# Optimization experiments

Measured on AMD Instinct MI355X. Metric: run time of the kernel, lower is better.

The kernel has to match this reference:

```python
import jax, jax.numpy as jnp
import numpy as np

N = 100000   # number of orientation vectors
MUL = 128    # multiplicity per output irrep


def _cg_tensors():
    # Clebsch-Gordan (wigner-3j style) tensors for 1o x 1o -> 0e, 1e, 2e
    # l=1 basis in e3nn real-SH order: index 0=y, 1=z, 2=x
    Y, Z, X = 0, 1, 2
    # l_out = 0: identity / sqrt(3)
    c0 = np.zeros((3, 3, 1), np.float32)
    for i in range(3):
        c0[i, i, 0] = 1.0 / np.sqrt(3.0)
    # l_out = 1: Levi-Civita / sqrt(6) (cyclic in (y,z,x) = cyclic in (x,y,z))
    c1 = np.zeros((3, 3, 3), np.float32)
    s = 1.0 / np.sqrt(6.0)
    for (i, j, k) in [(0, 1, 2), (1, 2, 0), (2, 0, 1)]:
        c1[i, j, k] = s
        c1[j, i, k] = -s
    # l_out = 2: symmetric traceless part, m = -2..2 -> (xy, yz, 2z^2-x^2-y^2, zx, x^2-y^2)
    a = 1.0 / np.sqrt(10.0)
    c2 = np.zeros((3, 3, 5), np.float32)
    c2[X, Y, 0] = c2[Y, X, 0] = a
    c2[Y, Z, 1] = c2[Z, Y, 1] = a
    c2[Z, Z, 2] = 2.0 * a / np.sqrt(3.0)
    c2[Y, Y, 2] = -a / np.sqrt(3.0)
    c2[X, X, 2] = -a / np.sqrt(3.0)
    c2[Z, X, 3] = c2[X, Z, 3] = a
    c2[X, X, 4] = a
    c2[Y, Y, 4] = -a
    return jnp.asarray(c0), jnp.asarray(c1), jnp.asarray(c2)

_CG = _cg_tensors()
# e3nn path weights: irrep_normalization='component', path_normalization='element'
# -> alpha = (2*l_out+1) / (mul1*mul2) = 2l+1, coefficient = sqrt(alpha)
_PW = (1.0, 3.0 ** 0.5, 5.0 ** 0.5)


def setup_inputs() -> dict:
    key = jax.random.key(0)
    k1, k2 = jax.random.split(key)
    ori = jax.random.normal(k1, (N, 3), dtype=jnp.float32)
    weights = jax.random.normal(k2, (3 * MUL,), dtype=jnp.float32)
    return {"ori": ori, "weights": weights}


def reference(ori, weights):
    # TensorProduct(1o, 1o -> 128x0e+128x1e+128x2e), 'uvw' paths, shared weights.
    w = weights.reshape(3, MUL)  # one (1,1,MUL) weight block per path
    n = ori.shape[0]
    outs = []
    for p, (cg, pw) in enumerate(zip(_CG, _PW)):
        t = jnp.einsum('ni,nj,ijk->nk', ori, ori, cg)      # [N, 2l+1]
        blk = pw * jnp.einsum('nk,w->nwk', t, w[p])        # [N, MUL, 2l+1]
        outs.append(blk.reshape(n, -1))
    return jnp.concatenate(outs, axis=-1)  # [N, MUL*(1+3+5)]
```

## Files before the change

kernel.cpp:

```cpp
#include <hip/hip_runtime.h>


#define THREADS 256
#define CPR 144
#define GRID 2016
#define RPT 28

__global__ __launch_bounds__(THREADS) void ori_embed_kernel(
    const float* __restrict__ ori,
    const float* __restrict__ weights,
    float* __restrict__ out,
    int n_rows)
{
    const int tid = blockIdx.x * THREADS + threadIdx.x;
    const int c = tid % CPR;
    const int g = tid / CPR;
    const int r0 = g * RPT;

    float coef[8];
    int sel[8];
#pragma unroll
    for (int i = 0; i < 8; ++i) {
        const int col = (i < 4) ? (4 * c + i) : (576 + 4 * c + (i - 4));
        if (col < 128)      { coef[i] = weights[col];  sel[i] = 0; }
        else if (col < 512) { coef[i] = 0.0f;          sel[i] = 0; }
        else { const int j = col - 512;
               coef[i] = weights[256 + j / 5];         sel[i] = 1 + j % 5; }
    }

    float4* __restrict__ out4 = reinterpret_cast<float4*>(out);

    if (r0 + RPT <= n_rows) {
        union { float4 v[RPT * 3 / 4]; float f[RPT * 3]; } d;
        const float4* __restrict__ src =
            reinterpret_cast<const float4*>(ori + 3 * (size_t)r0);
#pragma unroll
        for (int k = 0; k < RPT * 3 / 4; ++k) d.v[k] = src[k];

#pragma unroll
        for (int j = 0; j < RPT; ++j) {
            const float vy = d.f[3 * j + 0];
            const float vz = d.f[3 * j + 1];
            const float vx = d.f[3 * j + 2];
            const float xx = vx * vx, yy = vy * vy, zz = vz * vz;
            const float s0 = (xx + yy + zz) * 0.57735026918962576f;
            const float s1 = 1.41421356237309505f * (vx * vy);
            const float s2 = 1.41421356237309505f * (vy * vz);
            const float s3 = 0.40824829046386302f * (2.0f * zz - xx - yy);
            const float s4 = 1.41421356237309505f * (vz * vx);
            const float s5 = 0.70710678118654752f * (xx - yy);

            float r[8];
#pragma unroll
            for (int i = 0; i < 8; ++i) {
                float t = s0;
                t = (sel[i] == 1) ? s1 : t;
                t = (sel[i] == 2) ? s2 : t;
                t = (sel[i] == 3) ? s3 : t;
                t = (sel[i] == 4) ? s4 : t;
                t = (sel[i] == 5) ? s5 : t;
                r[i] = coef[i] * t;
            }
            const size_t base = (size_t)(r0 + j) * (2 * CPR) + c;
            out4[base]       = make_float4(r[0], r[1], r[2], r[3]);
            out4[base + CPR] = make_float4(r[4], r[5], r[6], r[7]);
        }
    } else {
        for (int j = 0; r0 + j < n_rows; ++j) {
            const int n = r0 + j;
            const float vy = ori[3 * n + 0];
            const float vz = ori[3 * n + 1];
            const float vx = ori[3 * n + 2];
            const float xx = vx * vx, yy = vy * vy, zz = vz * vz;
            const float s0 = (xx + yy + zz) * 0.57735026918962576f;
            const float s1 = 1.41421356237309505f * (vx * vy);
            const float s2 = 1.41421356237309505f * (vy * vz);
            const float s3 = 0.40824829046386302f * (2.0f * zz - xx - yy);
            const float s4 = 1.41421356237309505f * (vz * vx);
            const float s5 = 0.70710678118654752f * (xx - yy);

            float r[8];
#pragma unroll
            for (int i = 0; i < 8; ++i) {
                float t = s0;
                t = (sel[i] == 1) ? s1 : t;
                t = (sel[i] == 2) ? s2 : t;
                t = (sel[i] == 3) ? s3 : t;
                t = (sel[i] == 4) ? s4 : t;
                t = (sel[i] == 5) ? s5 : t;
                r[i] = coef[i] * t;
            }
            const size_t base = (size_t)n * (2 * CPR) + c;
            out4[base]       = make_float4(r[0], r[1], r[2], r[3]);
            out4[base + CPR] = make_float4(r[4], r[5], r[6], r[7]);
        }
    }
}

extern "C" void kernel_launch(void* const* d_in, const int* in_sizes, int n_in,
                              void* d_out, int out_size, void* d_ws, size_t ws_size,
                              hipStream_t stream) {
    const float* ori = (const float*)d_in[0];
    const float* weights = (const float*)d_in[1];
    float* out = (float*)d_out;
    const int n_rows = in_sizes[0] / 3;

    hipLaunchKernelGGL(ori_embed_kernel, dim3(GRID), dim3(THREADS), 0, stream,
                       ori, weights, out, n_rows);
}
```

Measured before the change: 93.38 us.

## Software-pipeline input loads in batches and double rows per thread group

Each thread group now handles 56 rows instead of 28, processed in batches of 8 rows. The next batch's input is prefetched into registers while the current batch computes and stores. This halves the grid and adds a launch-bounds occupancy hint, with the aim of lowering register pressure from the large unrolled load and overlapping reads with the write stream. The kernel is dominated by output writes, so the gain may be small, and fewer, larger groups risk load imbalance or lower parallelism.

```diff
diff --git a/kernel.cpp b/kernel.cpp
--- a/kernel.cpp
+++ b/kernel.cpp
@@ -3,10 +3,38 @@
 
 #define THREADS 256
 #define CPR 144
-#define GRID 2016
-#define RPT 28
+#define GRID 1017
+#define BATCH 8
+#define NB 7
+#define RPG (BATCH * NB)
 
-__global__ __launch_bounds__(THREADS) void ori_embed_kernel(
+__device__ __forceinline__ void emit_row(float4* __restrict__ out4, int n, int c,
+                                         float vy, float vz, float vx,
+                                         const float coef[8], const int sel[8]) {
+    const float xx = vx * vx, yy = vy * vy, zz = vz * vz;
+    const float s0 = (xx + yy + zz) * 0.57735026918962576f;
+    const float s1 = 1.41421356237309505f * (vx * vy);
+    const float s2 = 1.41421356237309505f * (vy * vz);
+    const float s3 = 0.40824829046386302f * (2.0f * zz - xx - yy);
+    const float s4 = 1.41421356237309505f * (vz * vx);
+    const float s5 = 0.70710678118654752f * (xx - yy);
+    float r[8];
+#pragma unroll
+    for (int i = 0; i < 8; ++i) {
+        float t = s0;
+        t = (sel[i] == 1) ? s1 : t;
+        t = (sel[i] == 2) ? s2 : t;
+        t = (sel[i] == 3) ? s3 : t;
+        t = (sel[i] == 4) ? s4 : t;
+        t = (sel[i] == 5) ? s5 : t;
+        r[i] = coef[i] * t;
+    }
+    const size_t ob = (size_t)n * (2 * CPR) + c;
+    out4[ob]       = make_float4(r[0], r[1], r[2], r[3]);
+    out4[ob + CPR] = make_float4(r[4], r[5], r[6], r[7]);
+}
+
+__global__ __launch_bounds__(THREADS, 4) void ori_embed_kernel(
     const float* __restrict__ ori,
     const float* __restrict__ weights,
     float* __restrict__ out,
@@ -15,7 +43,8 @@
     const int tid = blockIdx.x * THREADS + threadIdx.x;
     const int c = tid % CPR;
     const int g = tid / CPR;
-    const int r0 = g * RPT;
+    const int r0 = g * RPG;
+    if (r0 >= n_rows) return;
 
     float coef[8];
     int sel[8];
@@ -29,71 +58,39 @@
     }
 
     float4* __restrict__ out4 = reinterpret_cast<float4*>(out);
+    const float4* __restrict__ src = reinterpret_cast<const float4*>(ori);
 
-    if (r0 + RPT <= n_rows) {
-        union { float4 v[RPT * 3 / 4]; float f[RPT * 3]; } d;
-        const float4* __restrict__ src =
-            reinterpret_cast<const float4*>(ori + 3 * (size_t)r0);
+    const int nb = min(NB, (n_rows - r0) / BATCH);
+    const int base = 42 * g;
+
+    float4 cur[6], nxt[6];
+    if (nb > 0) {
 #pragma unroll
-        for (int k = 0; k < RPT * 3 / 4; ++k) d.v[k] = src[k];
+        for (int k = 0; k < 6; ++k) cur[k] = src[base + k];
+    }
+    for (int b = 0; b < nb; ++b) {
+        const bool more = (b + 1 < nb);
+        if (more) {
+#pragma unroll
+            for (int k = 0; k < 6; ++k) nxt[k] = src[base + 6 * (b + 1) + k];
+        }
+        const float* f = reinterpret_cast<const float*>(cur);
+        const int rb = r0 + b * BATCH;
+#pragma unroll
+        for (int j = 0; j < BATCH; ++j) {
+            emit_row(out4, rb + j, c, f[3 * j + 0], f[3 * j + 1], f[3 * j + 2],
+                     coef, sel);
+        }
+        if (more) {
+#pragma unroll
+            for (int k = 0; k < 6; ++k) cur[k] = nxt[k];
+        }
+    }
 
-#pragma unroll
-        for (int j = 0; j < RPT; ++j) {
-            const float vy = d.f[3 * j + 0];
-            const float vz = d.f[3 * j + 1];
-            const float vx = d.f[3 * j + 2];
-            const float xx = vx * vx, yy = vy * vy, zz = vz * vz;
-            const float s0 = (xx + yy + zz) * 0.57735026918962576f;
-            const float s1 = 1.41421356237309505f * (vx * vy);
-            const float s2 = 1.41421356237309505f * (vy * vz);
-            const float s3 = 0.40824829046386302f * (2.0f * zz - xx - yy);
-            const float s4 = 1.41421356237309505f * (vz * vx);
-            const float s5 = 0.70710678118654752f * (xx - yy);
-
-            float r[8];
-#pragma unroll
-            for (int i = 0; i < 8; ++i) {
-                float t = s0;
-                t = (sel[i] == 1) ? s1 : t;
-                t = (sel[i] == 2) ? s2 : t;
-                t = (sel[i] == 3) ? s3 : t;
-                t = (sel[i] == 4) ? s4 : t;
-                t = (sel[i] == 5) ? s5 : t;
-                r[i] = coef[i] * t;
-            }
-            const size_t base = (size_t)(r0 + j) * (2 * CPR) + c;
-            out4[base]       = make_float4(r[0], r[1], r[2], r[3]);
-            out4[base + CPR] = make_float4(r[4], r[5], r[6], r[7]);
-        }
-    } else {
-        for (int j = 0; r0 + j < n_rows; ++j) {
-            const int n = r0 + j;
-            const float vy = ori[3 * n + 0];
-            const float vz = ori[3 * n + 1];
-            const float vx = ori[3 * n + 2];
-            const float xx = vx * vx, yy = vy * vy, zz = vz * vz;
-            const float s0 = (xx + yy + zz) * 0.57735026918962576f;
-            const float s1 = 1.41421356237309505f * (vx * vy);
-            const float s2 = 1.41421356237309505f * (vy * vz);
-            const float s3 = 0.40824829046386302f * (2.0f * zz - xx - yy);
-            const float s4 = 1.41421356237309505f * (vz * vx);
-            const float s5 = 0.70710678118654752f * (xx - yy);
-
-            float r[8];
-#pragma unroll
-            for (int i = 0; i < 8; ++i) {
-                float t = s0;
-                t = (sel[i] == 1) ? s1 : t;
-                t = (sel[i] == 2) ? s2 : t;
-                t = (sel[i] == 3) ? s3 : t;
-                t = (sel[i] == 4) ? s4 : t;
-                t = (sel[i] == 5) ? s5 : t;
-                r[i] = coef[i] * t;
-            }
-            const size_t base = (size_t)n * (2 * CPR) + c;
-            out4[base]       = make_float4(r[0], r[1], r[2], r[3]);
-            out4[base + CPR] = make_float4(r[4], r[5], r[6], r[7]);
-        }
+    const int rend = min(r0 + RPG, n_rows);
+    for (int n = r0 + nb * BATCH; n < rend; ++n) {
+        emit_row(out4, n, c, ori[3 * n + 0], ori[3 * n + 1], ori[3 * n + 2],
+                 coef, sel);
     }
 }
 
```

Result: no change. 94.20 us (+0.9%).

## Stage output tiles in double-buffered LDS for fully contiguous streaming stores

Applied to the files above, without the earlier changes.

Output rows are now built in a double-buffered shared-memory tile of 8 rows by 288 float4 chunks. The block then copies each tile to global memory as one contiguous span, so consecutive threads write consecutive float4s. Each block processes 25 tiles, and computing the next tile overlaps with storing the current one. The goal is more coalesced, sequential write traffic in this store-bound kernel. The cost is extra LDS traffic, a barrier per tile, scalar per-thread loads of ori, and a serial tail loop in the last block.

```diff
diff --git a/kernel.cpp b/kernel.cpp
--- a/kernel.cpp
+++ b/kernel.cpp
@@ -1,10 +1,12 @@
 #include <hip/hip_runtime.h>
 
 
-#define THREADS 256
-#define CPR 144
-#define GRID 2016
-#define RPT 28
+#define THREADS 576
+#define GRID 512
+#define TPB 25
+#define TROWS 8
+#define CPRow 288
+#define TCHUNKS (TROWS * CPRow)
 
 __global__ __launch_bounds__(THREADS) void ori_embed_kernel(
     const float* __restrict__ ori,
@@ -12,16 +14,17 @@
     float* __restrict__ out,
     int n_rows)
 {
-    const int tid = blockIdx.x * THREADS + threadIdx.x;
-    const int c = tid % CPR;
-    const int g = tid / CPR;
-    const int r0 = g * RPT;
+    __shared__ float4 lds[2][TCHUNKS];
 
-    float coef[8];
-    int sel[8];
+    const int t = threadIdx.x;
+    const int c = t % CPRow;
+    const int ro = t / CPRow;
+
+    float coef[4];
+    int sel[4];
 #pragma unroll
-    for (int i = 0; i < 8; ++i) {
-        const int col = (i < 4) ? (4 * c + i) : (576 + 4 * c + (i - 4));
+    for (int i = 0; i < 4; ++i) {
+        const int col = 4 * c + i;
         if (col < 128)      { coef[i] = weights[col];  sel[i] = 0; }
         else if (col < 512) { coef[i] = 0.0f;          sel[i] = 0; }
         else { const int j = col - 512;
@@ -29,45 +32,15 @@
     }
 
     float4* __restrict__ out4 = reinterpret_cast<float4*>(out);
+    const int NT = n_rows / TROWS;
+    const int ti0 = blockIdx.x * TPB;
+    const int ti1 = min(ti0 + TPB, NT);
 
-    if (r0 + RPT <= n_rows) {
-        union { float4 v[RPT * 3 / 4]; float f[RPT * 3]; } d;
-        const float4* __restrict__ src =
-            reinterpret_cast<const float4*>(ori + 3 * (size_t)r0);
+    auto compute = [&](int ti, int kk) {
+        const int rbase = ti * TROWS + ro;
 #pragma unroll
-        for (int k = 0; k < RPT * 3 / 4; ++k) d.v[k] = src[k];
-
-#pragma unroll
-        for (int j = 0; j < RPT; ++j) {
-            const float vy = d.f[3 * j + 0];
-            const float vz = d.f[3 * j + 1];
-            const float vx = d.f[3 * j + 2];
-            const float xx = vx * vx, yy = vy * vy, zz = vz * vz;
-            const float s0 = (xx + yy + zz) * 0.57735026918962576f;
-            const float s1 = 1.41421356237309505f * (vx * vy);
-            const float s2 = 1.41421356237309505f * (vy * vz);
-            const float s3 = 0.40824829046386302f * (2.0f * zz - xx - yy);
-            const float s4 = 1.41421356237309505f * (vz * vx);
-            const float s5 = 0.70710678118654752f * (xx - yy);
-
-            float r[8];
-#pragma unroll
-            for (int i = 0; i < 8; ++i) {
-                float t = s0;
-                t = (sel[i] == 1) ? s1 : t;
-                t = (sel[i] == 2) ? s2 : t;
-                t = (sel[i] == 3) ? s3 : t;
-                t = (sel[i] == 4) ? s4 : t;
-                t = (sel[i] == 5) ? s5 : t;
-                r[i] = coef[i] * t;
-            }
-            const size_t base = (size_t)(r0 + j) * (2 * CPR) + c;
-            out4[base]       = make_float4(r[0], r[1], r[2], r[3]);
-            out4[base + CPR] = make_float4(r[4], r[5], r[6], r[7]);
-        }
-    } else {
-        for (int j = 0; r0 + j < n_rows; ++j) {
-            const int n = r0 + j;
+        for (int p = 0; p < 4; ++p) {
+            const int n = rbase + 2 * p;
             const float vy = ori[3 * n + 0];
             const float vz = ori[3 * n + 1];
             const float vx = ori[3 * n + 2];
@@ -78,21 +51,61 @@
             const float s3 = 0.40824829046386302f * (2.0f * zz - xx - yy);
             const float s4 = 1.41421356237309505f * (vz * vx);
             const float s5 = 0.70710678118654752f * (xx - yy);
+            float r[4];
+#pragma unroll
+            for (int i = 0; i < 4; ++i) {
+                float v = s0;
+                v = (sel[i] == 1) ? s1 : v;
+                v = (sel[i] == 2) ? s2 : v;
+                v = (sel[i] == 3) ? s3 : v;
+                v = (sel[i] == 4) ? s4 : v;
+                v = (sel[i] == 5) ? s5 : v;
+                r[i] = coef[i] * v;
+            }
+            lds[kk][(ro + 2 * p) * CPRow + c] = make_float4(r[0], r[1], r[2], r[3]);
+        }
+    };
 
-            float r[8];
+    if (ti0 < ti1) {
+        compute(ti0, 0);
+        __syncthreads();
+        int k = 0;
+        for (int ti = ti0; ti < ti1; ++ti, k ^= 1) {
+            if (ti + 1 < ti1) compute(ti + 1, k ^ 1);
+            const size_t gb = (size_t)ti * TCHUNKS;
 #pragma unroll
-            for (int i = 0; i < 8; ++i) {
-                float t = s0;
-                t = (sel[i] == 1) ? s1 : t;
-                t = (sel[i] == 2) ? s2 : t;
-                t = (sel[i] == 3) ? s3 : t;
-                t = (sel[i] == 4) ? s4 : t;
-                t = (sel[i] == 5) ? s5 : t;
-                r[i] = coef[i] * t;
+            for (int p = 0; p < 4; ++p) {
+                const int idx = p * THREADS + t;
+                out4[gb + idx] = lds[k][idx];
             }
-            const size_t base = (size_t)n * (2 * CPR) + c;
-            out4[base]       = make_float4(r[0], r[1], r[2], r[3]);
-            out4[base + CPR] = make_float4(r[4], r[5], r[6], r[7]);
+            __syncthreads();
+        }
+    }
+
+    if (blockIdx.x == GRID - 1 && ro == 0) {
+        for (int n = NT * TROWS; n < n_rows; ++n) {
+            const float vy = ori[3 * n + 0];
+            const float vz = ori[3 * n + 1];
+            const float vx = ori[3 * n + 2];
+            const float xx = vx * vx, yy = vy * vy, zz = vz * vz;
+            const float s0 = (xx + yy + zz) * 0.57735026918962576f;
+            const float s1 = 1.41421356237309505f * (vx * vy);
+            const float s2 = 1.41421356237309505f * (vy * vz);
+            const float s3 = 0.40824829046386302f * (2.0f * zz - xx - yy);
+            const float s4 = 1.41421356237309505f * (vz * vx);
+            const float s5 = 0.70710678118654752f * (xx - yy);
+            float r[4];
+#pragma unroll
+            for (int i = 0; i < 4; ++i) {
+                float v = s0;
+                v = (sel[i] == 1) ? s1 : v;
+                v = (sel[i] == 2) ? s2 : v;
+                v = (sel[i] == 3) ? s3 : v;
+                v = (sel[i] == 4) ? s4 : v;
+                v = (sel[i] == 5) ? s5 : v;
+                r[i] = coef[i] * v;
+            }
+            out4[(size_t)n * CPRow + c] = make_float4(r[0], r[1], r[2], r[3]);
         }
     }
 }
```

Result: slower. 113.2 us (+21.3%).
